# Kernel tuning notes

Hardware: AMD Instinct MI355X
Metric: run time of the kernel (lower is better)

Reference implementation:

```python
import jax, jax.numpy as jnp
import numpy as np

B, T, D = 2, 2048, 1024
H, G = 16, 4
HD = D // H          # 64 head dim
HPG = H // G         # 4 heads per group
EPS = 1e-5


def _layernorm(x, g, b):
    m = jnp.mean(x, axis=-1, keepdims=True)
    v = jnp.var(x, axis=-1, keepdims=True)
    return g * (x - m) / jnp.sqrt(v + EPS) + b


def setup_inputs() -> dict:
    key = jax.random.key(0)
    ks = jax.random.split(key, 8)
    s = lambda fan_in: 1.0 / np.sqrt(fan_in)
    return {
        "x": jax.random.normal(ks[0], (B, T, D), jnp.float32),
        "g1": jnp.ones((D,), jnp.float32),
        "bt1": jnp.zeros((D,), jnp.float32),
        "wq": jax.random.normal(ks[1], (D, D), jnp.float32) * s(D),
        "bq": jnp.zeros((D,), jnp.float32),
        "wk": jax.random.normal(ks[2], (D, G * HD), jnp.float32) * s(D),
        "bk": jnp.zeros((G * HD,), jnp.float32),
        "wv": jax.random.normal(ks[3], (D, G * HD), jnp.float32) * s(D),
        "bv": jnp.zeros((G * HD,), jnp.float32),
        "wo": jax.random.normal(ks[4], (D, D), jnp.float32) * s(D),
        "bo": jnp.zeros((D,), jnp.float32),
        "g2": jnp.ones((D,), jnp.float32),
        "bt2": jnp.zeros((D,), jnp.float32),
        "w1": jax.random.normal(ks[5], (D, 4 * D), jnp.float32) * s(D),
        "b1": jnp.zeros((4 * D,), jnp.float32),
        "w2": jax.random.normal(ks[6], (4 * D, D), jnp.float32) * s(4 * D),
        "b2": jnp.zeros((D,), jnp.float32),
    }


def reference(x, g1, bt1, wq, bq, wk, bk, wv, bv, wo, bo, g2, bt2, w1, b1, w2, b2):
    # pre-norm GQA causal attention (eval mode: dropout = identity)
    h = _layernorm(x, g1, bt1)
    q = (h @ wq + bq).reshape(B, T, G, HPG, HD)   # head i -> group i // HPG
    k = (h @ wk + bk).reshape(B, T, G, HD)
    v = (h @ wv + bv).reshape(B, T, G, HD)
    scores = jnp.einsum('bqgph,bkgh->bgpqk', q, k) / np.sqrt(HD).astype(np.float32)
    causal = jnp.triu(jnp.ones((T, T), bool), 1)
    scores = jnp.where(causal, -jnp.inf, scores)
    attn = jax.nn.softmax(scores, axis=-1)
    out = jnp.einsum('bgpqk,bkgh->bqgph', attn, v).reshape(B, T, D)
    x = x + out @ wo + bo
    # pre-norm GELU FFN (exact erf GELU, matching torch nn.GELU default)
    h2 = _layernorm(x, g2, bt2)
    f = jax.nn.gelu(h2 @ w1 + b1, approximate=False) @ w2 + b2
    return x + f
```

## Files before the change

kernel.cpp:

```cpp
#include <hip/hip_runtime.h>
#include <hip/hip_bf16.h>
#include <math.h>

constexpr int Dm = 1024;
constexpr int Tt = 2048;
constexpr int NB = 2;
constexpr int NROWS = NB * Tt;

#define LN_EPS 1e-5f

typedef __attribute__((ext_vector_type(4))) float f32x4;
typedef __attribute__((ext_vector_type(8))) short short8;

__device__ __forceinline__ unsigned short f2bf(float f) {
    unsigned int u = __builtin_bit_cast(unsigned int, f);
    u += 0x7fffu + ((u >> 16) & 1u);
    return (unsigned short)(u >> 16);
}
__device__ __forceinline__ float bf2f(unsigned short u) {
    unsigned int v = (unsigned int)u << 16;
    return __builtin_bit_cast(float, v);
}

__device__ __forceinline__ float gelu_exact(float v) {
    return 0.5f * v * (1.0f + erff(v * 0.70710678118654752f));
}

__device__ __forceinline__ void gload_lds16(const void* g, void* l) {
    __builtin_amdgcn_global_load_lds(
        (const __attribute__((address_space(1))) unsigned int*)g,
        (__attribute__((address_space(3))) unsigned int*)l, 16, 0, 0);
}

__global__ __launch_bounds__(256) void ln_kernel(const float* __restrict__ x,
        const float* __restrict__ gamma, const float* __restrict__ beta,
        unsigned short* __restrict__ out) {
    const int row = blockIdx.x;
    const int t = threadIdx.x;
    const float* xr = x + (size_t)row * Dm;
    float4 v = *(const float4*)(xr + t * 4);
    float s  = v.x + v.y + v.z + v.w;
    float s2 = v.x * v.x + v.y * v.y + v.z * v.z + v.w * v.w;
    #pragma unroll
    for (int off = 32; off > 0; off >>= 1) {
        s  += __shfl_down(s, off);
        s2 += __shfl_down(s2, off);
    }
    __shared__ float red[8];
    const int wid = t >> 6, lane = t & 63;
    if (lane == 0) { red[wid] = s; red[wid + 4] = s2; }
    __syncthreads();
    if (t == 0) {
        float a = red[0] + red[1] + red[2] + red[3];
        float c = red[4] + red[5] + red[6] + red[7];
        float mean = a * (1.0f / Dm);
        red[0] = mean;
        red[4] = c * (1.0f / Dm) - mean * mean;
    }
    __syncthreads();
    const float mean = red[0];
    const float rstd = rsqrtf(red[4] + LN_EPS);
    float4 gv = *(const float4*)(gamma + t * 4);
    float4 bv = *(const float4*)(beta + t * 4);
    ushort4 o;
    o.x = f2bf((v.x - mean) * rstd * gv.x + bv.x);
    o.y = f2bf((v.y - mean) * rstd * gv.y + bv.y);
    o.z = f2bf((v.z - mean) * rstd * gv.z + bv.z);
    o.w = f2bf((v.w - mean) * rstd * gv.w + bv.w);
    *(ushort4*)(out + (size_t)row * Dm + t * 4) = o;
}

__global__ __launch_bounds__(256) void transpose_cvt(const float* __restrict__ W,
        unsigned short* __restrict__ Wt, int K, int N) {
    __shared__ float tile[64][65];
    const int k0 = blockIdx.x * 64, n0 = blockIdx.y * 64;
    const int t = threadIdx.x;
    const int r = t >> 2, c = t & 3;
    #pragma unroll
    for (int i = 0; i < 4; i++) {
        const int f4 = c + i * 4;
        *(float4*)&tile[r][f4 * 4] = *(const float4*)(W + (size_t)(k0 + r) * N + n0 + f4 * 4);
    }
    __syncthreads();
    #pragma unroll
    for (int i = 0; i < 4; i++) {
        const int kk = c * 16 + i * 4;
        ushort4 o;
        o.x = f2bf(tile[kk + 0][r]);
        o.y = f2bf(tile[kk + 1][r]);
        o.z = f2bf(tile[kk + 2][r]);
        o.w = f2bf(tile[kk + 3][r]);
        *(ushort4*)(Wt + (size_t)(n0 + r) * K + k0 + kk) = o;
    }
}

template<int EPI, typename OutT>
__global__ __launch_bounds__(256) void mgemm(
        const unsigned short* __restrict__ A,
        const unsigned short* __restrict__ Bt,
        const float* __restrict__ bias,
        const float* __restrict__ res,
        OutT* __restrict__ C,
        int M, int N, int K) {
    __shared__ __align__(16) unsigned short As[128 * 32];
    __shared__ __align__(16) unsigned short Bs[128 * 32];
    const int t = threadIdx.x;
    const int w = t >> 6, l = t & 63;
    const int wr = w >> 1, wc = w & 1;
    const int li = l & 15, lh = l >> 4;
    const int m0 = blockIdx.y * 128, n0 = blockIdx.x * 128;
    const int lrow = t >> 2, lseg = t & 3;
    const unsigned short* Ag = A  + (size_t)(m0 + lrow) * K + lseg * 8;
    const unsigned short* Bg = Bt + (size_t)(n0 + lrow) * K + lseg * 8;
    unsigned short* Asw = As + w * 512;
    unsigned short* Bsw = Bs + w * 512;
    f32x4 acc[4][4] = {};
    for (int k0 = 0; k0 < K; k0 += 32) {
        __syncthreads();
        gload_lds16(Ag + k0, Asw);
        gload_lds16(Ag + (size_t)64 * K + k0, Asw + 2048);
        gload_lds16(Bg + k0, Bsw);
        gload_lds16(Bg + (size_t)64 * K + k0, Bsw + 2048);
        __syncthreads();
        short8 af[4], bfr[4];
        #pragma unroll
        for (int m = 0; m < 4; m++)
            af[m] = *(const short8*)&As[(wr * 64 + m * 16 + li) * 32 + lh * 8];
        #pragma unroll
        for (int n = 0; n < 4; n++)
            bfr[n] = *(const short8*)&Bs[(wc * 64 + n * 16 + li) * 32 + lh * 8];
        #pragma unroll
        for (int m = 0; m < 4; m++)
            #pragma unroll
            for (int n = 0; n < 4; n++)
                acc[m][n] = __builtin_amdgcn_mfma_f32_16x16x32_bf16(af[m], bfr[n], acc[m][n], 0, 0, 0);
    }
    #pragma unroll
    for (int n = 0; n < 4; n++) {
        const int col = n0 + wc * 64 + n * 16 + li;
        const float bv = bias[col];
        #pragma unroll
        for (int m = 0; m < 4; m++) {
            const int rbase = m0 + wr * 64 + m * 16 + lh * 4;
            #pragma unroll
            for (int q = 0; q < 4; q++) {
                const size_t idx = (size_t)(rbase + q) * N + col;
                float v = acc[m][n][q] + bv;
                if (EPI == 1) v += res[idx];
                if (EPI == 2) v = gelu_exact(v);
                if constexpr (sizeof(OutT) == 2) C[idx] = (OutT)f2bf(v);
                else                             C[idx] = v;
            }
        }
    }
}

__global__ __launch_bounds__(256) void attn_mfma(
        const unsigned short* __restrict__ qb,
        const unsigned short* __restrict__ kb,
        const unsigned short* __restrict__ vb,
        unsigned short* __restrict__ ob) {
    const int blk = blockIdx.x;
    const int qt = 31 - (blk & 31);
    const int head = (blk >> 5) & 15;
    const int b = blk >> 9;
    const int g = head >> 2;
    const int t = threadIdx.x;
    const int w = t >> 6, l = t & 63;
    const int li = l & 15, lh = l >> 4;
    const int sw = (li & 7) << 3;

    __shared__ __align__(16) unsigned short Ks[64 * 64];
    __shared__ __align__(16) unsigned short Vt[64 * 64];
    __shared__ __align__(16) unsigned short Pl[4][16 * 64];

    unsigned short* Pw = Pl[w];

    short8 aq[2];
    {
        const unsigned short* qrow =
            qb + (size_t)(b * Tt + qt * 64 + w * 16 + li) * Dm + head * 64;
        #pragma unroll
        for (int s = 0; s < 2; s++) {
            uint4 raw = *(const uint4*)(qrow + s * 32 + lh * 8);
            unsigned short* u = (unsigned short*)&raw;
            #pragma unroll
            for (int j = 0; j < 8; j++) u[j] = f2bf(bf2f(u[j]) * 0.125f);
            aq[s] = *(const short8*)&raw;
        }
    }

    float mrow[4], lrow[4];
    f32x4 acc[4] = {};
    #pragma unroll
    for (int r = 0; r < 4; r++) { mrow[r] = -INFINITY; lrow[r] = 0.0f; }

    const unsigned short* kgb = kb + (size_t)(b * Tt) * 256 + g * 64;
    const unsigned short* vgb = vb + (size_t)(b * Tt) * 256 + g * 64;
    const int skey = t >> 3, sseg = t & 7;

    for (int kt = 0; kt <= qt; kt++) {
        __syncthreads();
        #pragma unroll
        for (int i = 0; i < 2; i++) {
            const int key = i * 32 + skey;
            const size_t gro = (size_t)(kt * 64 + key) * 256 + sseg * 8;
            uint4 k4 = *(const uint4*)(kgb + gro);
            *(uint4*)&Ks[key * 64 + ((sseg * 8) ^ ((key & 7) << 3))] = k4;
            uint4 v4 = *(const uint4*)(vgb + gro);
            const unsigned short* vp = (const unsigned short*)&v4;
            #pragma unroll
            for (int j = 0; j < 8; j++) {
                const int dim = sseg * 8 + j;
                Vt[dim * 64 + (key ^ (j << 3))] = vp[j];
            }
        }
        __syncthreads();

        const bool diagt = (kt == qt);
        f32x4 s4[4];
        #pragma unroll
        for (int tile = 0; tile < 4; tile++)
            s4[tile] = (f32x4){-INFINITY, -INFINITY, -INFINITY, -INFINITY};
        #pragma unroll
        for (int tile = 0; tile < 4; tile++) {
            if (diagt && tile > w) continue;
            f32x4 z = {};
            #pragma unroll
            for (int s = 0; s < 2; s++) {
                short8 bk = *(const short8*)
                    &Ks[(tile * 16 + li) * 64 + ((s * 32 + lh * 8) ^ sw)];
                z = __builtin_amdgcn_mfma_f32_16x16x32_bf16(aq[s], bk, z, 0, 0, 0);
            }
            if (diagt && tile == w) {
                #pragma unroll
                for (int r = 0; r < 4; r++)
                    if (li > lh * 4 + r) z[r] = -INFINITY;
            }
            s4[tile] = z;
        }
        float mx[4];
        #pragma unroll
        for (int r = 0; r < 4; r++) {
            float v = s4[0][r];
            v = fmaxf(v, s4[1][r]); v = fmaxf(v, s4[2][r]); v = fmaxf(v, s4[3][r]);
            mx[r] = v;
        }
        #pragma unroll
        for (int off = 1; off < 16; off <<= 1)
            #pragma unroll
            for (int r = 0; r < 4; r++)
                mx[r] = fmaxf(mx[r], __shfl_xor(mx[r], off));
        float corr[4];
        #pragma unroll
        for (int r = 0; r < 4; r++) {
            const float nm = fmaxf(mrow[r], mx[r]);
            corr[r] = __expf(mrow[r] - nm);
            mrow[r] = nm;
        }
        float p[4][4], rs[4] = {};
        #pragma unroll
        for (int tile = 0; tile < 4; tile++)
            #pragma unroll
            for (int r = 0; r < 4; r++) {
                const float pv = __expf(s4[tile][r] - mrow[r]);
                p[tile][r] = pv;
                rs[r] += pv;
            }
        #pragma unroll
        for (int off = 1; off < 16; off <<= 1)
            #pragma unroll
            for (int r = 0; r < 4; r++)
                rs[r] += __shfl_xor(rs[r], off);
        #pragma unroll
        for (int r = 0; r < 4; r++)
            lrow[r] = lrow[r] * corr[r] + rs[r];
        #pragma unroll
        for (int n = 0; n < 4; n++)
            #pragma unroll
            for (int r = 0; r < 4; r++)
                acc[n][r] *= corr[r];
        #pragma unroll
        for (int tile = 0; tile < 4; tile++)
            #pragma unroll
            for (int r = 0; r < 4; r++) {
                const int q = lh * 4 + r;
                Pw[q * 64 + ((tile * 16 + li) ^ ((q & 7) << 3))] = f2bf(p[tile][r]);
            }
        #pragma unroll
        for (int s = 0; s < 2; s++) {
            short8 pa = *(const short8*)&Pw[li * 64 + ((s * 32 + lh * 8) ^ sw)];
            #pragma unroll
            for (int n = 0; n < 4; n++) {
                short8 bv = *(const short8*)
                    &Vt[(n * 16 + li) * 64 + ((s * 32 + lh * 8) ^ sw)];
                acc[n] = __builtin_amdgcn_mfma_f32_16x16x32_bf16(pa, bv, acc[n], 0, 0, 0);
            }
        }
    }
    float inv[4];
    #pragma unroll
    for (int r = 0; r < 4; r++) inv[r] = 1.0f / lrow[r];
    unsigned short* orow =
        ob + (size_t)(b * Tt + qt * 64 + w * 16) * Dm + head * 64;
    #pragma unroll
    for (int n = 0; n < 4; n++)
        #pragma unroll
        for (int r = 0; r < 4; r++)
            orow[(size_t)(lh * 4 + r) * Dm + n * 16 + li] = f2bf(acc[n][r] * inv[r]);
}

extern "C" void kernel_launch(void* const* d_in, const int* in_sizes, int n_in,
                              void* d_out, int out_size, void* d_ws, size_t ws_size,
                              hipStream_t stream) {
    (void)in_sizes; (void)n_in; (void)out_size; (void)ws_size;
    const float* x   = (const float*)d_in[0];
    const float* g1  = (const float*)d_in[1];
    const float* bt1 = (const float*)d_in[2];
    const float* wq  = (const float*)d_in[3];
    const float* bq  = (const float*)d_in[4];
    const float* wk  = (const float*)d_in[5];
    const float* bk  = (const float*)d_in[6];
    const float* wv  = (const float*)d_in[7];
    const float* bv  = (const float*)d_in[8];
    const float* wo  = (const float*)d_in[9];
    const float* bo  = (const float*)d_in[10];
    const float* g2  = (const float*)d_in[11];
    const float* bt2 = (const float*)d_in[12];
    const float* w1  = (const float*)d_in[13];
    const float* b1  = (const float*)d_in[14];
    const float* w2  = (const float*)d_in[15];
    const float* b2  = (const float*)d_in[16];
    float* out = (float*)d_out;

    char* p = (char*)d_ws;
    unsigned short* h_bf  = (unsigned short*)p; p += (size_t)NROWS * Dm * 2;
    unsigned short* h2_bf = (unsigned short*)p; p += (size_t)NROWS * Dm * 2;
    unsigned short* at_bf = (unsigned short*)p; p += (size_t)NROWS * Dm * 2;
    unsigned short* f1_bf = (unsigned short*)p; p += (size_t)NROWS * 4096 * 2;
    unsigned short* q_bf  = (unsigned short*)p; p += (size_t)NROWS * 1024 * 2;
    unsigned short* k_bf  = (unsigned short*)p; p += (size_t)NROWS * 256 * 2;
    unsigned short* v_bf  = (unsigned short*)p; p += (size_t)NROWS * 256 * 2;
    unsigned short* wqT = (unsigned short*)p; p += (size_t)1024 * 1024 * 2;
    unsigned short* wkT = (unsigned short*)p; p += (size_t)256 * 1024 * 2;
    unsigned short* wvT = (unsigned short*)p; p += (size_t)256 * 1024 * 2;
    unsigned short* woT = (unsigned short*)p; p += (size_t)1024 * 1024 * 2;
    unsigned short* w1T = (unsigned short*)p; p += (size_t)4096 * 1024 * 2;
    unsigned short* w2T = (unsigned short*)p; p += (size_t)1024 * 4096 * 2;

    transpose_cvt<<<dim3(16, 16), 256, 0, stream>>>(wq, wqT, 1024, 1024);
    transpose_cvt<<<dim3(16, 4),  256, 0, stream>>>(wk, wkT, 1024, 256);
    transpose_cvt<<<dim3(16, 4),  256, 0, stream>>>(wv, wvT, 1024, 256);
    transpose_cvt<<<dim3(16, 16), 256, 0, stream>>>(wo, woT, 1024, 1024);
    transpose_cvt<<<dim3(16, 64), 256, 0, stream>>>(w1, w1T, 1024, 4096);
    transpose_cvt<<<dim3(64, 16), 256, 0, stream>>>(w2, w2T, 4096, 1024);

    ln_kernel<<<NROWS, 256, 0, stream>>>(x, g1, bt1, h_bf);
    mgemm<0, unsigned short><<<dim3(8, 32), 256, 0, stream>>>(h_bf, wqT, bq, nullptr, q_bf, NROWS, 1024, 1024);
    mgemm<0, unsigned short><<<dim3(2, 32), 256, 0, stream>>>(h_bf, wkT, bk, nullptr, k_bf, NROWS, 256, 1024);
    mgemm<0, unsigned short><<<dim3(2, 32), 256, 0, stream>>>(h_bf, wvT, bv, nullptr, v_bf, NROWS, 256, 1024);
    attn_mfma<<<NB * 16 * (Tt / 64), 256, 0, stream>>>(q_bf, k_bf, v_bf, at_bf);
    mgemm<1, float><<<dim3(8, 32), 256, 0, stream>>>(at_bf, woT, bo, x, out, NROWS, 1024, 1024);
    ln_kernel<<<NROWS, 256, 0, stream>>>(out, g2, bt2, h2_bf);
    mgemm<2, unsigned short><<<dim3(32, 32), 256, 0, stream>>>(h2_bf, w1T, b1, nullptr, f1_bf, NROWS, 4096, 1024);
    mgemm<1, float><<<dim3(8, 32), 256, 0, stream>>>(f1_bf, w2T, b2, out, out, NROWS, 1024, 4096);
}
```

Baseline: 572.0 us.

## Fuse Q/K projections, pre-transpose V, double-buffer attention tiles, add BN=64 GEMM tiles

Merges the Q and K projection GEMMs into one launch over concatenated weights and biases. The V GEMM now writes V transposed, so attention no longer does a scalar LDS transpose. Attention double-buffers its K/V tiles with async global-to-LDS loads, overlapping the next tile's fetch with compute. The GEMM also gains a 128x64 tile variant, used for the narrower-N GEMMs to raise block counts, at the cost of less data reuse per block.

```diff
diff --git a/kernel.cpp b/kernel.cpp
--- a/kernel.cpp
+++ b/kernel.cpp
@@ -94,7 +94,14 @@
     }
 }
 
-template<int EPI, typename OutT>
+__global__ __launch_bounds__(256) void concat_bias(const float* __restrict__ bq,
+        const float* __restrict__ bk, float* __restrict__ bqk) {
+    const int i = blockIdx.x * 256 + threadIdx.x;
+    if (i < 1024) bqk[i] = bq[i];
+    else if (i < 1280) bqk[i] = bk[i - 1024];
+}
+
+template<int EPI, int BN, typename OutT>
 __global__ __launch_bounds__(256) void mgemm(
         const unsigned short* __restrict__ A,
         const unsigned short* __restrict__ Bt,
@@ -103,34 +110,38 @@
         OutT* __restrict__ C,
         int M, int N, int K) {
     __shared__ __align__(16) unsigned short As[128 * 32];
-    __shared__ __align__(16) unsigned short Bs[128 * 32];
+    __shared__ __align__(16) unsigned short Bs[BN * 32];
+    constexpr int MR = (BN == 128) ? 4 : 2;
+    constexpr int WM = (BN == 128) ? 64 : 32;
     const int t = threadIdx.x;
     const int w = t >> 6, l = t & 63;
-    const int wr = w >> 1, wc = w & 1;
+    const int wr = (BN == 128) ? (w >> 1) : w;
+    const int wc = (BN == 128) ? (w & 1) : 0;
     const int li = l & 15, lh = l >> 4;
-    const int m0 = blockIdx.y * 128, n0 = blockIdx.x * 128;
+    const int m0 = blockIdx.y * 128, n0 = blockIdx.x * BN;
     const int lrow = t >> 2, lseg = t & 3;
     const unsigned short* Ag = A  + (size_t)(m0 + lrow) * K + lseg * 8;
     const unsigned short* Bg = Bt + (size_t)(n0 + lrow) * K + lseg * 8;
     unsigned short* Asw = As + w * 512;
     unsigned short* Bsw = Bs + w * 512;
-    f32x4 acc[4][4] = {};
+    f32x4 acc[MR][4] = {};
     for (int k0 = 0; k0 < K; k0 += 32) {
         __syncthreads();
         gload_lds16(Ag + k0, Asw);
         gload_lds16(Ag + (size_t)64 * K + k0, Asw + 2048);
         gload_lds16(Bg + k0, Bsw);
-        gload_lds16(Bg + (size_t)64 * K + k0, Bsw + 2048);
+        if constexpr (BN == 128)
+            gload_lds16(Bg + (size_t)64 * K + k0, Bsw + 2048);
         __syncthreads();
-        short8 af[4], bfr[4];
-        #pragma unroll
-        for (int m = 0; m < 4; m++)
-            af[m] = *(const short8*)&As[(wr * 64 + m * 16 + li) * 32 + lh * 8];
+        short8 af[MR], bfr[4];
+        #pragma unroll
+        for (int m = 0; m < MR; m++)
+            af[m] = *(const short8*)&As[(wr * WM + m * 16 + li) * 32 + lh * 8];
         #pragma unroll
         for (int n = 0; n < 4; n++)
             bfr[n] = *(const short8*)&Bs[(wc * 64 + n * 16 + li) * 32 + lh * 8];
         #pragma unroll
-        for (int m = 0; m < 4; m++)
+        for (int m = 0; m < MR; m++)
             #pragma unroll
             for (int n = 0; n < 4; n++)
                 acc[m][n] = __builtin_amdgcn_mfma_f32_16x16x32_bf16(af[m], bfr[n], acc[m][n], 0, 0, 0);
@@ -140,25 +151,30 @@
         const int col = n0 + wc * 64 + n * 16 + li;
         const float bv = bias[col];
         #pragma unroll
-        for (int m = 0; m < 4; m++) {
-            const int rbase = m0 + wr * 64 + m * 16 + lh * 4;
+        for (int m = 0; m < MR; m++) {
+            const int rbase = m0 + wr * WM + m * 16 + lh * 4;
             #pragma unroll
             for (int q = 0; q < 4; q++) {
-                const size_t idx = (size_t)(rbase + q) * N + col;
+                const int row = rbase + q;
                 float v = acc[m][n][q] + bv;
-                if (EPI == 1) v += res[idx];
-                if (EPI == 2) v = gelu_exact(v);
-                if constexpr (sizeof(OutT) == 2) C[idx] = (OutT)f2bf(v);
-                else                             C[idx] = v;
+                if (EPI == 3) {
+                    const size_t tidx = ((size_t)((row >> 11) * 256 + col)) * 2048 + (row & 2047);
+                    C[tidx] = (OutT)f2bf(v);
+                } else {
+                    const size_t idx = (size_t)row * N + col;
+                    if (EPI == 1) v += res[idx];
+                    if (EPI == 2) v = gelu_exact(v);
+                    if constexpr (sizeof(OutT) == 2) C[idx] = (OutT)f2bf(v);
+                    else                             C[idx] = v;
+                }
             }
         }
     }
 }
 
 __global__ __launch_bounds__(256) void attn_mfma(
-        const unsigned short* __restrict__ qb,
-        const unsigned short* __restrict__ kb,
-        const unsigned short* __restrict__ vb,
+        const unsigned short* __restrict__ qkb,
+        const unsigned short* __restrict__ vtb,
         unsigned short* __restrict__ ob) {
     const int blk = blockIdx.x;
     const int qt = 31 - (blk & 31);
@@ -170,16 +186,15 @@
     const int li = l & 15, lh = l >> 4;
     const int sw = (li & 7) << 3;
 
-    __shared__ __align__(16) unsigned short Ks[64 * 64];
-    __shared__ __align__(16) unsigned short Vt[64 * 64];
+    __shared__ __align__(16) unsigned short Ks[2][64 * 64];
+    __shared__ __align__(16) unsigned short Vt[2][64 * 64];
     __shared__ __align__(16) unsigned short Pl[4][16 * 64];
-
     unsigned short* Pw = Pl[w];
 
     short8 aq[2];
     {
         const unsigned short* qrow =
-            qb + (size_t)(b * Tt + qt * 64 + w * 16 + li) * Dm + head * 64;
+            qkb + (size_t)(b * Tt + qt * 64 + w * 16 + li) * 1280 + head * 64;
         #pragma unroll
         for (int s = 0; s < 2; s++) {
             uint4 raw = *(const uint4*)(qrow + s * 32 + lh * 8);
@@ -195,27 +210,30 @@
     #pragma unroll
     for (int r = 0; r < 4; r++) { mrow[r] = -INFINITY; lrow[r] = 0.0f; }
 
-    const unsigned short* kgb = kb + (size_t)(b * Tt) * 256 + g * 64;
-    const unsigned short* vgb = vb + (size_t)(b * Tt) * 256 + g * 64;
-    const int skey = t >> 3, sseg = t & 7;
+    const int srow = l >> 3, sseg = l & 7;
+    const unsigned short* kg = qkb + (size_t)b * Tt * 1280 + 1024 + g * 64;
+    const unsigned short* vg = vtb + (size_t)((b * 4 + g) * 64) * 2048;
+
+    auto stage = [&](int buf, int tile) {
+        #pragma unroll
+        for (int c = 0; c < 2; c++) {
+            const int rb = (c * 4 + w) * 8;
+            const int kr = rb + srow;
+            const int sg = (sseg ^ (kr & 7)) * 8;
+            gload_lds16(kg + (size_t)(tile * 64 + kr) * 1280 + sg, &Ks[buf][rb * 64]);
+            gload_lds16(vg + (size_t)kr * 2048 + tile * 64 + sg,   &Vt[buf][rb * 64]);
+        }
+    };
+
+    stage(0, 0);
+    asm volatile("s_waitcnt vmcnt(0)" ::: "memory");
+    __builtin_amdgcn_s_barrier();
 
     for (int kt = 0; kt <= qt; kt++) {
-        __syncthreads();
-        #pragma unroll
-        for (int i = 0; i < 2; i++) {
-            const int key = i * 32 + skey;
-            const size_t gro = (size_t)(kt * 64 + key) * 256 + sseg * 8;
-            uint4 k4 = *(const uint4*)(kgb + gro);
-            *(uint4*)&Ks[key * 64 + ((sseg * 8) ^ ((key & 7) << 3))] = k4;
-            uint4 v4 = *(const uint4*)(vgb + gro);
-            const unsigned short* vp = (const unsigned short*)&v4;
-            #pragma unroll
-            for (int j = 0; j < 8; j++) {
-                const int dim = sseg * 8 + j;
-                Vt[dim * 64 + (key ^ (j << 3))] = vp[j];
-            }
-        }
-        __syncthreads();
+        const int cur = kt & 1;
+        if (kt < qt) stage(cur ^ 1, kt + 1);
+        const unsigned short* KsB = Ks[cur];
+        const unsigned short* VtB = Vt[cur];
 
         const bool diagt = (kt == qt);
         f32x4 s4[4];
@@ -229,7 +247,7 @@
             #pragma unroll
             for (int s = 0; s < 2; s++) {
                 short8 bk = *(const short8*)
-                    &Ks[(tile * 16 + li) * 64 + ((s * 32 + lh * 8) ^ sw)];
+                    &KsB[(tile * 16 + li) * 64 + ((s * 32 + lh * 8) ^ sw)];
                 z = __builtin_amdgcn_mfma_f32_16x16x32_bf16(aq[s], bk, z, 0, 0, 0);
             }
             if (diagt && tile == w) {
@@ -293,10 +311,12 @@
             #pragma unroll
             for (int n = 0; n < 4; n++) {
                 short8 bv = *(const short8*)
-                    &Vt[(n * 16 + li) * 64 + ((s * 32 + lh * 8) ^ sw)];
+                    &VtB[(n * 16 + li) * 64 + ((s * 32 + lh * 8) ^ sw)];
                 acc[n] = __builtin_amdgcn_mfma_f32_16x16x32_bf16(pa, bv, acc[n], 0, 0, 0);
             }
         }
+        asm volatile("s_waitcnt vmcnt(0)" ::: "memory");
+        __builtin_amdgcn_s_barrier();
     }
     float inv[4];
     #pragma unroll
@@ -338,30 +358,29 @@
     unsigned short* h2_bf = (unsigned short*)p; p += (size_t)NROWS * Dm * 2;
     unsigned short* at_bf = (unsigned short*)p; p += (size_t)NROWS * Dm * 2;
     unsigned short* f1_bf = (unsigned short*)p; p += (size_t)NROWS * 4096 * 2;
-    unsigned short* q_bf  = (unsigned short*)p; p += (size_t)NROWS * 1024 * 2;
-    unsigned short* k_bf  = (unsigned short*)p; p += (size_t)NROWS * 256 * 2;
-    unsigned short* v_bf  = (unsigned short*)p; p += (size_t)NROWS * 256 * 2;
-    unsigned short* wqT = (unsigned short*)p; p += (size_t)1024 * 1024 * 2;
-    unsigned short* wkT = (unsigned short*)p; p += (size_t)256 * 1024 * 2;
-    unsigned short* wvT = (unsigned short*)p; p += (size_t)256 * 1024 * 2;
-    unsigned short* woT = (unsigned short*)p; p += (size_t)1024 * 1024 * 2;
-    unsigned short* w1T = (unsigned short*)p; p += (size_t)4096 * 1024 * 2;
-    unsigned short* w2T = (unsigned short*)p; p += (size_t)1024 * 4096 * 2;
-
-    transpose_cvt<<<dim3(16, 16), 256, 0, stream>>>(wq, wqT, 1024, 1024);
-    transpose_cvt<<<dim3(16, 4),  256, 0, stream>>>(wk, wkT, 1024, 256);
+    unsigned short* qk_bf = (unsigned short*)p; p += (size_t)NROWS * 1280 * 2;
+    unsigned short* vt_bf = (unsigned short*)p; p += (size_t)512 * 2048 * 2;
+    unsigned short* wqkT = (unsigned short*)p; p += (size_t)1280 * 1024 * 2;
+    unsigned short* wvT  = (unsigned short*)p; p += (size_t)256 * 1024 * 2;
+    unsigned short* woT  = (unsigned short*)p; p += (size_t)1024 * 1024 * 2;
+    unsigned short* w1T  = (unsigned short*)p; p += (size_t)4096 * 1024 * 2;
+    unsigned short* w2T  = (unsigned short*)p; p += (size_t)1024 * 4096 * 2;
+    float* bqk = (float*)p; p += 1280 * 4;
+
+    transpose_cvt<<<dim3(16, 16), 256, 0, stream>>>(wq, wqkT, 1024, 1024);
+    transpose_cvt<<<dim3(16, 4),  256, 0, stream>>>(wk, wqkT + (size_t)1024 * 1024, 1024, 256);
     transpose_cvt<<<dim3(16, 4),  256, 0, stream>>>(wv, wvT, 1024, 256);
     transpose_cvt<<<dim3(16, 16), 256, 0, stream>>>(wo, woT, 1024, 1024);
     transpose_cvt<<<dim3(16, 64), 256, 0, stream>>>(w1, w1T, 1024, 4096);
     transpose_cvt<<<dim3(64, 16), 256, 0, stream>>>(w2, w2T, 4096, 1024);
+    concat_bias<<<5, 256, 0, stream>>>(bq, bk, bqk);
 
     ln_kernel<<<NROWS, 256, 0, stream>>>(x, g1, bt1, h_bf);
-    mgemm<0, unsigned short><<<dim3(8, 32), 256, 0, stream>>>(h_bf, wqT, bq, nullptr, q_bf, NROWS, 1024, 1024);
-    mgemm<0, unsigned short><<<dim3(2, 32), 256, 0, stream>>>(h_bf, wkT, bk, nullptr, k_bf, NROWS, 256, 1024);
-    mgemm<0, unsigned short><<<dim3(2, 32), 256, 0, stream>>>(h_bf, wvT, bv, nullptr, v_bf, NROWS, 256, 1024);
-    attn_mfma<<<NB * 16 * (Tt / 64), 256, 0, stream>>>(q_bf, k_bf, v_bf, at_bf);
-    mgemm<1, float><<<dim3(8, 32), 256, 0, stream>>>(at_bf, woT, bo, x, out, NROWS, 1024, 1024);
+    mgemm<0, 64, unsigned short><<<dim3(20, 32), 256, 0, stream>>>(h_bf, wqkT, bqk, nullptr, qk_bf, NROWS, 1280, 1024);
+    mgemm<3, 64, unsigned short><<<dim3(4, 32), 256, 0, stream>>>(h_bf, wvT, bv, nullptr, vt_bf, NROWS, 256, 1024);
+    attn_mfma<<<NB * 16 * (Tt / 64), 256, 0, stream>>>(qk_bf, vt_bf, at_bf);
+    mgemm<1, 64, float><<<dim3(16, 32), 256, 0, stream>>>(at_bf, woT, bo, x, out, NROWS, 1024, 1024);
     ln_kernel<<<NROWS, 256, 0, stream>>>(out, g2, bt2, h2_bf);
-    mgemm<2, unsigned short><<<dim3(32, 32), 256, 0, stream>>>(h2_bf, w1T, b1, nullptr, f1_bf, NROWS, 4096, 1024);
-    mgemm<1, float><<<dim3(8, 32), 256, 0, stream>>>(f1_bf, w2T, b2, out, out, NROWS, 1024, 4096);
-}
+    mgemm<2, 128, unsigned short><<<dim3(32, 32), 256, 0, stream>>>(h2_bf, w1T, b1, nullptr, f1_bf, NROWS, 4096, 1024);
+    mgemm<1, 64, float><<<dim3(16, 32), 256, 0, stream>>>(f1_bf, w2T, b2, out, out, NROWS, 1024, 4096);
+}
```

Result: faster. 492.9 us (-13.8%).
